# Kernel optimization log

Hardware: AMD Instinct MI355X
Metric: run time of the kernel (lower is better)

The kernel has to match this reference:

```python
import jax, jax.numpy as jnp
import numpy as np

B, H, W = 8, 64, 64
D = 256          # in_dim == key_dim == value_dim
HEADS = 8
DK = D // HEADS  # per-head channels (key == value)
EPS = 1e-5


def _ln(x, g, b):
    m = jnp.mean(x, axis=-1, keepdims=True)
    v = jnp.var(x, axis=-1, keepdims=True)
    return (x - m) * jax.lax.rsqrt(v + EPS) * g + b


def setup_inputs() -> dict:
    key = jax.random.key(0)
    ks = jax.random.split(key, 8)
    return {
        "x1": jax.random.normal(ks[0], (B, H, W, 2 * D), jnp.float32),
        "x2": jax.random.normal(ks[1], (B, H, W, D), jnp.float32),
        "linear_w": jax.random.normal(ks[2], (2 * D, D), jnp.float32) * 0.02,
        "linear_b": jax.random.normal(ks[3], (D,), jnp.float32) * 0.02,
        "ln1_g": jnp.ones((D,), jnp.float32) + jax.random.normal(ks[4], (D,), jnp.float32) * 0.02,
        "ln1_b": jax.random.normal(ks[5], (D,), jnp.float32) * 0.02,
        "reproj_w": jax.random.normal(ks[6], (2 * D, D), jnp.float32) * 0.02,  # 1x1 conv kernel [out,in]
        "reproj_b": jax.random.normal(ks[7], (2 * D,), jnp.float32) * 0.02,
        "ln_attn_g": jnp.ones((2 * D,), jnp.float32),
        "ln_attn_b": jnp.zeros((2 * D,), jnp.float32),
    }


def _cross_attention(n1, n2, reproj_w, reproj_b, ln_g, ln_b):
    # n1 (values source), n2 (keys/queries source): [B,H,W,D]
    N = H * W
    v = n1.reshape(B, N, D).transpose(0, 2, 1).reshape(B, HEADS, DK, N)
    kq = n2.reshape(B, N, D).transpose(0, 2, 1).reshape(B, HEADS, DK, N)
    k = jax.nn.softmax(kq, axis=-1)  # softmax over tokens (dim=2 in torch slice)
    q = jax.nn.softmax(kq, axis=2)   # softmax over per-head channels (dim=1 in torch slice)
    # attended[b,h,d,n] = sum_m sum_e q[b,h,d,m] k[b,h,e,m] v[b,h,e,n]
    ctx = jnp.einsum('bhdm,bhem->bhde', q, k)          # [B,h,dk,dk]
    att = jnp.einsum('bhde,bhen->bhdn', ctx, v)        # [B,h,dk,N]
    agg = att.reshape(B, D, H, W)                      # concat heads along channels
    rep = jnp.einsum('od,bdhw->bohw', reproj_w, agg) + reproj_b[None, :, None, None]
    rep = rep.transpose(0, 2, 3, 1)                    # [B,H,W,2D]
    return _ln(rep, ln_g, ln_b)


def reference(x1, x2, linear_w, linear_b, ln1_g, ln1_b, reproj_w, reproj_b, ln_attn_g, ln_attn_b):
    n1 = _ln(x1 @ linear_w + linear_b, ln1_g, ln1_b)   # [B,H,W,D]
    n2 = _ln(x2, ln1_g, ln1_b)                          # [B,H,W,D]
    attn = _cross_attention(n1, n2, reproj_w, reproj_b, ln_attn_g, ln_attn_b)
    return x1 + attn
```

## Files before the change

kernel.cpp:

```cpp
#include <hip/hip_runtime.h>
#include <stdint.h>

typedef __bf16 bf16x8 __attribute__((ext_vector_type(8)));
typedef float f32x4 __attribute__((ext_vector_type(4)));

#define EPS 1e-5f

__device__ __forceinline__ float b2f(unsigned short u) {
    union { unsigned int i; float f; } c; c.i = ((unsigned int)u) << 16; return c.f;
}
__device__ __forceinline__ unsigned short f2b(float f) {
    union { float f; unsigned int i; } c; c.f = f;
    unsigned int i = c.i;
    return (unsigned short)((i + 0x7FFFu + ((i >> 16) & 1u)) >> 16);
}

__global__ void k_zero(float* __restrict__ p, int n) {
    int i = blockIdx.x * 256 + threadIdx.x;
    if (i < n) p[i] = 0.0f;
}

__global__ void k_params(const float* __restrict__ lw, const float* __restrict__ rw,
                         const float* __restrict__ lb, const float* __restrict__ g1,
                         const float* __restrict__ b1, const float* __restrict__ rb,
                         const float* __restrict__ ga, const float* __restrict__ ba,
                         unsigned short* __restrict__ wt1,
                         unsigned short* __restrict__ rwb,
                         unsigned short* __restrict__ vec) {
    int gid = blockIdx.x * 256 + threadIdx.x;
    if (gid < 131072) {
        int k = gid >> 8, n = gid & 255;
        wt1[n * 512 + k] = f2b(lw[gid]);
    } else if (gid < 262144) {
        int j = gid - 131072;
        rwb[j] = f2b(rw[j]);
    } else if (gid < 264448) {
        int j = gid - 262144;
        if (j < 256)       vec[j] = f2b(lb[j]);
        else if (j < 512)  vec[j] = f2b(g1[j - 256]);
        else if (j < 768)  vec[j] = f2b(b1[j - 512]);
        else if (j < 1280) vec[j] = f2b(rb[j - 768]);
        else if (j < 1792) vec[j] = f2b(ga[j - 1280]);
        else               vec[j] = f2b(ba[j - 1792]);
    }
}

__global__ __launch_bounds__(256) void k_stats(const float* __restrict__ x2,
                                               float2* __restrict__ stats) {
    int t = threadIdx.x, lane = t & 63, w = t >> 6;
    size_t row = (size_t)blockIdx.x * 4 + w;
    float4 f = *(const float4*)(x2 + row * 256 + lane * 4);
    float s = f.x + f.y + f.z + f.w;
    float q = f.x * f.x + f.y * f.y + f.z * f.z + f.w * f.w;
#pragma unroll
    for (int msk = 1; msk < 64; msk <<= 1) {
        s += __shfl_xor(s, msk, 64);
        q += __shfl_xor(q, msk, 64);
    }
    float mn = s * (1.0f / 256.0f);
    float rstd = rsqrtf(q * (1.0f / 256.0f) - mn * mn + EPS);
    if (lane == 0) stats[row] = make_float2(mn, rstd);
}

__global__ __launch_bounds__(256) void k_ctx(const float* __restrict__ x2,
                                             const float2* __restrict__ stats,
                                             const unsigned short* __restrict__ vec,
                                             float* __restrict__ ctxraw) {
    __shared__ float E[64 * 36];
    __shared__ float Q[64 * 36];
    __shared__ float gs[32], bs[32];
    int bh = blockIdx.x >> 3;
    int b = bh >> 3, h = bh & 7;
    int ch = blockIdx.x & 7;
    int t = threadIdx.x;
    if (t < 32) { gs[t] = b2f(vec[256 + h * 32 + t]); bs[t] = b2f(vec[512 + h * 32 + t]); }
    __syncthreads();
    int d = t >> 3, e0 = (t & 7) * 4;
    float a0 = 0.f, a1 = 0.f, a2 = 0.f, a3 = 0.f;
    const float* base = x2 + ((size_t)b * 4096 + ch * 512) * 256 + h * 32;
    int srow = b * 4096 + ch * 512;
    const int m = t >> 2, c0 = (t & 3) * 8;
    for (int s0 = 0; s0 < 512; s0 += 64) {
        float2 st = stats[srow + s0 + m];
        const float4* p = (const float4*)(base + (size_t)(s0 + m) * 256 + c0);
        float4 f0 = p[0], f1 = p[1];
        float ev[8];
        ev[0] = __expf((f0.x - st.x) * st.y * gs[c0 + 0] + bs[c0 + 0]);
        ev[1] = __expf((f0.y - st.x) * st.y * gs[c0 + 1] + bs[c0 + 1]);
        ev[2] = __expf((f0.z - st.x) * st.y * gs[c0 + 2] + bs[c0 + 2]);
        ev[3] = __expf((f0.w - st.x) * st.y * gs[c0 + 3] + bs[c0 + 3]);
        ev[4] = __expf((f1.x - st.x) * st.y * gs[c0 + 4] + bs[c0 + 4]);
        ev[5] = __expf((f1.y - st.x) * st.y * gs[c0 + 5] + bs[c0 + 5]);
        ev[6] = __expf((f1.z - st.x) * st.y * gs[c0 + 6] + bs[c0 + 6]);
        ev[7] = __expf((f1.w - st.x) * st.y * gs[c0 + 7] + bs[c0 + 7]);
        float ps = ev[0] + ev[1] + ev[2] + ev[3] + ev[4] + ev[5] + ev[6] + ev[7];
        ps += __shfl_xor(ps, 1, 64);
        ps += __shfl_xor(ps, 2, 64);
        float qi = 1.0f / ps;
        *(float4*)(E + m * 36 + c0)     = make_float4(ev[0], ev[1], ev[2], ev[3]);
        *(float4*)(E + m * 36 + c0 + 4) = make_float4(ev[4], ev[5], ev[6], ev[7]);
        *(float4*)(Q + m * 36 + c0)     = make_float4(ev[0]*qi, ev[1]*qi, ev[2]*qi, ev[3]*qi);
        *(float4*)(Q + m * 36 + c0 + 4) = make_float4(ev[4]*qi, ev[5]*qi, ev[6]*qi, ev[7]*qi);
        __syncthreads();
#pragma unroll 4
        for (int mm = 0; mm < 64; mm++) {
            float qd = Q[mm * 36 + d];
            float4 e4 = *(const float4*)(E + mm * 36 + e0);
            a0 += qd * e4.x; a1 += qd * e4.y; a2 += qd * e4.z; a3 += qd * e4.w;
        }
        __syncthreads();
    }
    float* dst = ctxraw + ((size_t)bh << 10) + (d << 5) + e0;
    atomicAdd(dst + 0, a0);
    atomicAdd(dst + 1, a1);
    atomicAdd(dst + 2, a2);
    atomicAdd(dst + 3, a3);
}

__global__ __launch_bounds__(256) void k_w2(const float* __restrict__ ctxraw,
                                            const unsigned short* __restrict__ rwb,
                                            unsigned short* __restrict__ w2t) {
    __shared__ float ctx_s[1024];
    __shared__ float cinv[32];
    int blk = blockIdx.x;
    int b = blk >> 6, h = (blk >> 3) & 7, os = blk & 7;
    int bh = b * 8 + h;
    int t = threadIdx.x;
#pragma unroll
    for (int i = 0; i < 4; i++) ctx_s[t + 256 * i] = ctxraw[((size_t)bh << 10) + t + 256 * i];
    __syncthreads();
    if (t < 32) {
        float s = 0.f;
#pragma unroll
        for (int d = 0; d < 32; d++) s += ctx_s[d * 32 + t];
        cinv[t] = 1.0f / s;
    }
    __syncthreads();
    int o = os * 64 + (t >> 2);
    int e0 = (t & 3) * 8;
    float wv[32];
    const uint4* wp = (const uint4*)(rwb + (size_t)o * 256 + h * 32);
#pragma unroll
    for (int qd = 0; qd < 4; qd++) {
        uint4 u = wp[qd];
        unsigned int uu[4] = {u.x, u.y, u.z, u.w};
#pragma unroll
        for (int j = 0; j < 4; j++) {
            wv[qd * 8 + j * 2]     = b2f((unsigned short)(uu[j] & 0xFFFFu));
            wv[qd * 8 + j * 2 + 1] = b2f((unsigned short)(uu[j] >> 16));
        }
    }
    float s[8];
#pragma unroll
    for (int j = 0; j < 8; j++) s[j] = 0.f;
#pragma unroll 8
    for (int d = 0; d < 32; d++) {
        float w = wv[d];
#pragma unroll
        for (int j = 0; j < 8; j++) s[j] += ctx_s[d * 32 + e0 + j] * w;
    }
    ushort4 o4a, o4b;
    o4a.x = f2b(s[0] * cinv[e0 + 0]); o4a.y = f2b(s[1] * cinv[e0 + 1]);
    o4a.z = f2b(s[2] * cinv[e0 + 2]); o4a.w = f2b(s[3] * cinv[e0 + 3]);
    o4b.x = f2b(s[4] * cinv[e0 + 4]); o4b.y = f2b(s[5] * cinv[e0 + 5]);
    o4b.z = f2b(s[6] * cinv[e0 + 6]); o4b.w = f2b(s[7] * cinv[e0 + 7]);
    unsigned short* dst = w2t + ((size_t)b * 512 + o) * 256 + h * 32 + e0;
    *(ushort4*)dst = o4a;
    *(ushort4*)(dst + 4) = o4b;
}

__global__ __launch_bounds__(256) void k_gemm1(
    const float* __restrict__ x1, const unsigned short* __restrict__ wt1,
    const unsigned short* __restrict__ vec, unsigned short* __restrict__ n1) {
    __shared__ unsigned short pool[16896];
    unsigned short* As = pool;
    unsigned short* Bs = pool + 2560;
    unsigned short* n1s = pool;
    const int t = threadIdx.x;
    const int lane = t & 63, w = t >> 6;
    const int l15 = lane & 15, quad = lane >> 4;
    const int row0 = blockIdx.x * 64;
    const int mrow = (w << 4) + l15;
    const int k8 = quad * 8;
    const int stg_m = t >> 2, stg_k = (t & 3) * 8;

    f32x4 acc[16];
#pragma unroll
    for (int i = 0; i < 16; i++) acc[i] = (f32x4){0.f, 0.f, 0.f, 0.f};

    for (int k0 = 0; k0 < 512; k0 += 32) {
        {
            const float* xf = x1 + (size_t)(row0 + stg_m) * 512 + k0 + stg_k;
            float4 f0 = *(const float4*)xf;
            float4 f1 = *(const float4*)(xf + 4);
            ushort4 lo, hi;
            lo.x = f2b(f0.x); lo.y = f2b(f0.y); lo.z = f2b(f0.z); lo.w = f2b(f0.w);
            hi.x = f2b(f1.x); hi.y = f2b(f1.y); hi.z = f2b(f1.z); hi.w = f2b(f1.w);
            *(ushort4*)(As + stg_m * 40 + stg_k) = lo;
            *(ushort4*)(As + stg_m * 40 + stg_k + 4) = hi;
        }
#pragma unroll
        for (int p = 0; p < 4; p++) {
            int n = stg_m + p * 64;
            *(uint4*)(Bs + n * 40 + stg_k) =
                *(const uint4*)(wt1 + (size_t)n * 512 + k0 + stg_k);
        }
        __syncthreads();
        bf16x8 a = *(const bf16x8*)(As + mrow * 40 + k8);
#pragma unroll
        for (int cb = 0; cb < 16; cb++) {
            bf16x8 bf = *(const bf16x8*)(Bs + ((cb << 4) + l15) * 40 + k8);
            acc[cb] = __builtin_amdgcn_mfma_f32_16x16x32_bf16(a, bf, acc[cb], 0, 0, 0);
        }
        __syncthreads();
    }
#pragma unroll
    for (int cb = 0; cb < 16; cb++) {
        float bc = b2f(vec[(cb << 4) + l15]);
#pragma unroll
        for (int r = 0; r < 4; r++) acc[cb][r] += bc;
    }
    float mean_[4], rstd_[4];
#pragma unroll
    for (int r = 0; r < 4; r++) {
        float s = 0.f, q = 0.f;
#pragma unroll
        for (int cb = 0; cb < 16; cb++) { float v = acc[cb][r]; s += v; q += v * v; }
#pragma unroll
        for (int msk = 1; msk < 16; msk <<= 1) {
            s += __shfl_xor(s, msk, 64);
            q += __shfl_xor(q, msk, 64);
        }
        float mn = s * (1.0f / 256.0f);
        mean_[r] = mn;
        rstd_[r] = rsqrtf(q * (1.0f / 256.0f) - mn * mn + EPS);
    }
#pragma unroll
    for (int cb = 0; cb < 16; cb++) {
        int col = (cb << 4) + l15;
        float gg = b2f(vec[256 + col]), bbv = b2f(vec[512 + col]);
#pragma unroll
        for (int r = 0; r < 4; r++) {
            int rr = (w << 4) + (quad << 2) + r;
            n1s[rr * 264 + col] = f2b((acc[cb][r] - mean_[r]) * rstd_[r] * gg + bbv);
        }
    }
    __syncthreads();
    {
        int row = t >> 2;
        unsigned short* dst = n1 + (size_t)(row0 + row) * 256;
        const unsigned short* src = n1s + row * 264;
#pragma unroll
        for (int j = 0; j < 8; j++) {
            int chunk = (t & 3) * 8 + j;
            *(uint4*)(dst + chunk * 8) = *(const uint4*)(src + chunk * 8);
        }
    }
}

__global__ __launch_bounds__(512) void k_gemm2(
    const unsigned short* __restrict__ n1, const unsigned short* __restrict__ w2t,
    const unsigned short* __restrict__ vec, const float* __restrict__ x1,
    float* __restrict__ out) {
    __shared__ unsigned short As[64 * 40];
    __shared__ unsigned short Bs[512 * 40];
    __shared__ float2 red[2][64];
    const int t = threadIdx.x;
    const int lane = t & 63, w = t >> 6;
    const int l15 = lane & 15, quad = lane >> 4;
    const int hf = w >> 2, wr = w & 3;
    const int row0 = blockIdx.x * 64;
    const unsigned short* wb = w2t + (size_t)(row0 >> 12) * (512 * 256);
    const int mrow = (wr << 4) + l15;
    const int k8 = quad * 8;

    f32x4 acc[16];
#pragma unroll
    for (int i = 0; i < 16; i++) acc[i] = (f32x4){0.f, 0.f, 0.f, 0.f};

    for (int k0 = 0; k0 < 256; k0 += 32) {
        if (t < 256) {
            int m = t >> 2, kc = (t & 3) * 8;
            *(uint4*)(As + m * 40 + kc) =
                *(const uint4*)(n1 + (size_t)(row0 + m) * 256 + k0 + kc);
        }
#pragma unroll
        for (int p = 0; p < 4; p++) {
            int n = (t >> 2) + p * 128, kc = (t & 3) * 8;
            *(uint4*)(Bs + n * 40 + kc) =
                *(const uint4*)(wb + (size_t)n * 256 + k0 + kc);
        }
        __syncthreads();
        bf16x8 a = *(const bf16x8*)(As + mrow * 40 + k8);
#pragma unroll
        for (int cb = 0; cb < 16; cb++) {
            int ncol = (hf << 8) + (cb << 4) + l15;
            bf16x8 bf = *(const bf16x8*)(Bs + ncol * 40 + k8);
            acc[cb] = __builtin_amdgcn_mfma_f32_16x16x32_bf16(a, bf, acc[cb], 0, 0, 0);
        }
        __syncthreads();
    }
#pragma unroll
    for (int cb = 0; cb < 16; cb++) {
        float bc = b2f(vec[768 + (hf << 8) + (cb << 4) + l15]);
#pragma unroll
        for (int r = 0; r < 4; r++) acc[cb][r] += bc;
    }
#pragma unroll
    for (int r = 0; r < 4; r++) {
        float s = 0.f, q = 0.f;
#pragma unroll
        for (int cb = 0; cb < 16; cb++) { float v = acc[cb][r]; s += v; q += v * v; }
#pragma unroll
        for (int msk = 1; msk < 16; msk <<= 1) {
            s += __shfl_xor(s, msk, 64);
            q += __shfl_xor(q, msk, 64);
        }
        if (l15 == 0) red[hf][(wr << 4) + (quad << 2) + r] = make_float2(s, q);
    }
    __syncthreads();
    float mean_[4], rstd_[4];
#pragma unroll
    for (int r = 0; r < 4; r++) {
        int rl = (wr << 4) + (quad << 2) + r;
        float2 cA = red[0][rl], cB = red[1][rl];
        float s = cA.x + cB.x, q = cA.y + cB.y;
        float mn = s * (1.0f / 512.0f);
        mean_[r] = mn;
        rstd_[r] = rsqrtf(q * (1.0f / 512.0f) - mn * mn + EPS);
    }
#pragma unroll
    for (int cb = 0; cb < 16; cb++) {
        int col = (hf << 8) + (cb << 4) + l15;
        float gg = b2f(vec[1280 + col]), bbv = b2f(vec[1792 + col]);
#pragma unroll
        for (int r = 0; r < 4; r++) {
            size_t idx = (size_t)(row0 + (wr << 4) + (quad << 2) + r) * 512 + col;
            out[idx] = (acc[cb][r] - mean_[r]) * rstd_[r] * gg + bbv + x1[idx];
        }
    }
}

extern "C" void kernel_launch(void* const* d_in, const int* in_sizes, int n_in,
                              void* d_out, int out_size, void* d_ws, size_t ws_size,
                              hipStream_t stream) {
    const float* x1 = (const float*)d_in[0];
    const float* x2 = (const float*)d_in[1];
    const float* lw = (const float*)d_in[2];
    const float* lb = (const float*)d_in[3];
    const float* g1 = (const float*)d_in[4];
    const float* b1 = (const float*)d_in[5];
    const float* rw = (const float*)d_in[6];
    const float* rb = (const float*)d_in[7];
    const float* ga = (const float*)d_in[8];
    const float* ba = (const float*)d_in[9];
    float* out = (float*)d_out;

    char* ws = (char*)d_ws;
    float*          ctxr  = (float*)(ws);
    float2*         stats = (float2*)(ws + 262144);
    unsigned short* wt1   = (unsigned short*)(ws + 524288);
    unsigned short* rwb   = (unsigned short*)(ws + 786432);
    unsigned short* vec   = (unsigned short*)(ws + 1048576);
    unsigned short* w2t   = (unsigned short*)(ws + 1064960);
    unsigned short* n1    = (unsigned short*)(ws + 4194304);

    k_zero<<<dim3(256), dim3(256), 0, stream>>>(ctxr, 65536);
    k_params<<<dim3(1033), dim3(256), 0, stream>>>(lw, rw, lb, g1, b1, rb, ga, ba,
                                                   wt1, rwb, vec);
    k_stats<<<dim3(8192), dim3(256), 0, stream>>>(x2, stats);
    k_ctx<<<dim3(512), dim3(256), 0, stream>>>(x2, stats, vec, ctxr);
    k_w2<<<dim3(512), dim3(256), 0, stream>>>(ctxr, rwb, w2t);
    k_gemm1<<<dim3(512), dim3(256), 0, stream>>>(x1, wt1, vec, n1);
    k_gemm2<<<dim3(512), dim3(512), 0, stream>>>(n1, w2t, vec, x1, out);
}
```

Before: 244.0 us.

## Use MFMA for ctx, drop atomics, enlarge GEMM row tiles to 128

The ctx kernel now computes the per-head q·k^T product with 32x32x16 bf16 MFMA over token slabs instead of scalar FMAs. It writes per-chunk partial results that k_w2 sums, which removes the zero-fill kernel and the float atomics. Both GEMM kernels move to 128-row tiles with 512 threads, and gemm2 keeps the full 512-column row in one wave so the cross-wave LayerNorm reduction through shared memory is gone. The cost is bf16 rounding of the softmax terms in ctx and higher register pressure from 32 accumulators in gemm2.

```diff
diff --git a/kernel.cpp b/kernel.cpp
--- a/kernel.cpp
+++ b/kernel.cpp
@@ -3,6 +3,7 @@
 
 typedef __bf16 bf16x8 __attribute__((ext_vector_type(8)));
 typedef float f32x4 __attribute__((ext_vector_type(4)));
+typedef float f32x16 __attribute__((ext_vector_type(16)));
 
 #define EPS 1e-5f
 
@@ -13,11 +14,6 @@
     union { float f; unsigned int i; } c; c.f = f;
     unsigned int i = c.i;
     return (unsigned short)((i + 0x7FFFu + ((i >> 16) & 1u)) >> 16);
-}
-
-__global__ void k_zero(float* __restrict__ p, int n) {
-    int i = blockIdx.x * 256 + threadIdx.x;
-    if (i < n) p[i] = 0.0f;
 }
 
 __global__ void k_params(const float* __restrict__ lw, const float* __restrict__ rw,
@@ -65,59 +61,83 @@
 __global__ __launch_bounds__(256) void k_ctx(const float* __restrict__ x2,
                                              const float2* __restrict__ stats,
                                              const unsigned short* __restrict__ vec,
-                                             float* __restrict__ ctxraw) {
-    __shared__ float E[64 * 36];
-    __shared__ float Q[64 * 36];
-    __shared__ float gs[32], bs[32];
-    int bh = blockIdx.x >> 3;
-    int b = bh >> 3, h = bh & 7;
-    int ch = blockIdx.x & 7;
-    int t = threadIdx.x;
-    if (t < 32) { gs[t] = b2f(vec[256 + h * 32 + t]); bs[t] = b2f(vec[512 + h * 32 + t]); }
+                                             float* __restrict__ ctxr) {
+    __shared__ f32x4 pool4[1056];
+    unsigned short* E = (unsigned short*)pool4;
+    unsigned short* Q = E + 32 * 132;
+    float* Racc = (float*)pool4;
+
+    const int blk = blockIdx.x;
+    const int bh = blk >> 3, chunk = blk & 7;
+    const int b = bh >> 3, h = bh & 7;
+    const int t = threadIdx.x;
+    const int ch = t & 31, tk2 = t >> 5;
+    const int w = t >> 6, lane = t & 63;
+    const int khalf = lane >> 5, mn32 = lane & 31;
+
+    const float gch = b2f(vec[256 + h * 32 + ch]);
+    const float bch = b2f(vec[512 + h * 32 + ch]);
+    const int tokbase = b * 4096 + chunk * 512;
+    const float* xb = x2 + (size_t)tokbase * 256 + h * 32;
+
+    f32x16 acc = {};
+    for (int slab = 0; slab < 4; slab++) {
+#pragma unroll
+        for (int it = 0; it < 8; it++) {
+            int tl = it * 16 + tk2 * 2;
+            int tok = slab * 128 + tl;
+            float2 st0 = stats[tokbase + tok];
+            float2 st1 = stats[tokbase + tok + 1];
+            float xv0 = xb[(size_t)tok * 256 + ch];
+            float xv1 = xb[(size_t)(tok + 1) * 256 + ch];
+            float e0 = __expf((xv0 - st0.x) * st0.y * gch + bch);
+            float e1 = __expf((xv1 - st1.x) * st1.y * gch + bch);
+            float s0 = e0, s1 = e1;
+#pragma unroll
+            for (int msk = 1; msk < 32; msk <<= 1) {
+                s0 += __shfl_xor(s0, msk, 64);
+                s1 += __shfl_xor(s1, msk, 64);
+            }
+            float qi0 = 1.0f / s0, qi1 = 1.0f / s1;
+            unsigned int pe = (unsigned int)f2b(e0) | ((unsigned int)f2b(e1) << 16);
+            unsigned int pq = (unsigned int)f2b(e0 * qi0) | ((unsigned int)f2b(e1 * qi1) << 16);
+            *(unsigned int*)(E + ch * 132 + tl) = pe;
+            *(unsigned int*)(Q + ch * 132 + tl) = pq;
+        }
+        __syncthreads();
+#pragma unroll
+        for (int k16 = 0; k16 < 2; k16++) {
+            int off = mn32 * 132 + w * 32 + k16 * 16 + khalf * 8;
+            union { bf16x8 v; uint2 u[2]; } fa, fb;
+            fa.u[0] = *(const uint2*)(Q + off);
+            fa.u[1] = *(const uint2*)(Q + off + 4);
+            fb.u[0] = *(const uint2*)(E + off);
+            fb.u[1] = *(const uint2*)(E + off + 4);
+            acc = __builtin_amdgcn_mfma_f32_32x32x16_bf16(fa.v, fb.v, acc, 0, 0, 0);
+        }
+        __syncthreads();
+    }
+    {
+        float* R = Racc + w * 1024;
+#pragma unroll
+        for (int j = 0; j < 16; j++) {
+            int row = (j & 3) + 8 * (j >> 2) + 4 * khalf;
+            R[row * 32 + mn32] = acc[j];
+        }
+    }
     __syncthreads();
-    int d = t >> 3, e0 = (t & 7) * 4;
-    float a0 = 0.f, a1 = 0.f, a2 = 0.f, a3 = 0.f;
-    const float* base = x2 + ((size_t)b * 4096 + ch * 512) * 256 + h * 32;
-    int srow = b * 4096 + ch * 512;
-    const int m = t >> 2, c0 = (t & 3) * 8;
-    for (int s0 = 0; s0 < 512; s0 += 64) {
-        float2 st = stats[srow + s0 + m];
-        const float4* p = (const float4*)(base + (size_t)(s0 + m) * 256 + c0);
-        float4 f0 = p[0], f1 = p[1];
-        float ev[8];
-        ev[0] = __expf((f0.x - st.x) * st.y * gs[c0 + 0] + bs[c0 + 0]);
-        ev[1] = __expf((f0.y - st.x) * st.y * gs[c0 + 1] + bs[c0 + 1]);
-        ev[2] = __expf((f0.z - st.x) * st.y * gs[c0 + 2] + bs[c0 + 2]);
-        ev[3] = __expf((f0.w - st.x) * st.y * gs[c0 + 3] + bs[c0 + 3]);
-        ev[4] = __expf((f1.x - st.x) * st.y * gs[c0 + 4] + bs[c0 + 4]);
-        ev[5] = __expf((f1.y - st.x) * st.y * gs[c0 + 5] + bs[c0 + 5]);
-        ev[6] = __expf((f1.z - st.x) * st.y * gs[c0 + 6] + bs[c0 + 6]);
-        ev[7] = __expf((f1.w - st.x) * st.y * gs[c0 + 7] + bs[c0 + 7]);
-        float ps = ev[0] + ev[1] + ev[2] + ev[3] + ev[4] + ev[5] + ev[6] + ev[7];
-        ps += __shfl_xor(ps, 1, 64);
-        ps += __shfl_xor(ps, 2, 64);
-        float qi = 1.0f / ps;
-        *(float4*)(E + m * 36 + c0)     = make_float4(ev[0], ev[1], ev[2], ev[3]);
-        *(float4*)(E + m * 36 + c0 + 4) = make_float4(ev[4], ev[5], ev[6], ev[7]);
-        *(float4*)(Q + m * 36 + c0)     = make_float4(ev[0]*qi, ev[1]*qi, ev[2]*qi, ev[3]*qi);
-        *(float4*)(Q + m * 36 + c0 + 4) = make_float4(ev[4]*qi, ev[5]*qi, ev[6]*qi, ev[7]*qi);
-        __syncthreads();
-#pragma unroll 4
-        for (int mm = 0; mm < 64; mm++) {
-            float qd = Q[mm * 36 + d];
-            float4 e4 = *(const float4*)(E + mm * 36 + e0);
-            a0 += qd * e4.x; a1 += qd * e4.y; a2 += qd * e4.z; a3 += qd * e4.w;
-        }
-        __syncthreads();
-    }
-    float* dst = ctxraw + ((size_t)bh << 10) + (d << 5) + e0;
-    atomicAdd(dst + 0, a0);
-    atomicAdd(dst + 1, a1);
-    atomicAdd(dst + 2, a2);
-    atomicAdd(dst + 3, a3);
-}
-
-__global__ __launch_bounds__(256) void k_w2(const float* __restrict__ ctxraw,
+    {
+        float4 s = make_float4(0.f, 0.f, 0.f, 0.f);
+#pragma unroll
+        for (int ww = 0; ww < 4; ww++) {
+            float4 v = *(const float4*)(Racc + ww * 1024 + t * 4);
+            s.x += v.x; s.y += v.y; s.z += v.z; s.w += v.w;
+        }
+        *(float4*)(ctxr + ((size_t)(bh * 8 + chunk) << 10) + t * 4) = s;
+    }
+}
+
+__global__ __launch_bounds__(256) void k_w2(const float* __restrict__ ctxr,
                                             const unsigned short* __restrict__ rwb,
                                             unsigned short* __restrict__ w2t) {
     __shared__ float ctx_s[1024];
@@ -127,7 +147,13 @@
     int bh = b * 8 + h;
     int t = threadIdx.x;
 #pragma unroll
-    for (int i = 0; i < 4; i++) ctx_s[t + 256 * i] = ctxraw[((size_t)bh << 10) + t + 256 * i];
+    for (int i = 0; i < 4; i++) {
+        float s = 0.f;
+#pragma unroll
+        for (int c = 0; c < 8; c++)
+            s += ctxr[((size_t)(bh * 8 + c) << 10) + t + 256 * i];
+        ctx_s[t + 256 * i] = s;
+    }
     __syncthreads();
     if (t < 32) {
         float s = 0.f;
@@ -169,20 +195,20 @@
     *(ushort4*)(dst + 4) = o4b;
 }
 
-__global__ __launch_bounds__(256) void k_gemm1(
+__global__ __launch_bounds__(512, 2) void k_gemm1(
     const float* __restrict__ x1, const unsigned short* __restrict__ wt1,
     const unsigned short* __restrict__ vec, unsigned short* __restrict__ n1) {
-    __shared__ unsigned short pool[16896];
-    unsigned short* As = pool;
-    unsigned short* Bs = pool + 2560;
-    unsigned short* n1s = pool;
+    __shared__ f32x4 pool4[2112];
+    unsigned short* As = (unsigned short*)pool4;
+    unsigned short* Bs = As + 128 * 40;
+    unsigned short* n1s = (unsigned short*)pool4;
     const int t = threadIdx.x;
     const int lane = t & 63, w = t >> 6;
     const int l15 = lane & 15, quad = lane >> 4;
-    const int row0 = blockIdx.x * 64;
-    const int mrow = (w << 4) + l15;
+    const int row0 = blockIdx.x * 128;
+    const int mrow = w * 16 + l15;
     const int k8 = quad * 8;
-    const int stg_m = t >> 2, stg_k = (t & 3) * 8;
+    const int sm = t >> 2, sk = (t & 3) * 8;
 
     f32x4 acc[16];
 #pragma unroll
@@ -190,27 +216,27 @@
 
     for (int k0 = 0; k0 < 512; k0 += 32) {
         {
-            const float* xf = x1 + (size_t)(row0 + stg_m) * 512 + k0 + stg_k;
+            const float* xf = x1 + (size_t)(row0 + sm) * 512 + k0 + sk;
             float4 f0 = *(const float4*)xf;
             float4 f1 = *(const float4*)(xf + 4);
             ushort4 lo, hi;
             lo.x = f2b(f0.x); lo.y = f2b(f0.y); lo.z = f2b(f0.z); lo.w = f2b(f0.w);
             hi.x = f2b(f1.x); hi.y = f2b(f1.y); hi.z = f2b(f1.z); hi.w = f2b(f1.w);
-            *(ushort4*)(As + stg_m * 40 + stg_k) = lo;
-            *(ushort4*)(As + stg_m * 40 + stg_k + 4) = hi;
-        }
-#pragma unroll
-        for (int p = 0; p < 4; p++) {
-            int n = stg_m + p * 64;
-            *(uint4*)(Bs + n * 40 + stg_k) =
-                *(const uint4*)(wt1 + (size_t)n * 512 + k0 + stg_k);
+            *(ushort4*)(As + sm * 40 + sk) = lo;
+            *(ushort4*)(As + sm * 40 + sk + 4) = hi;
+        }
+#pragma unroll
+        for (int p = 0; p < 2; p++) {
+            int n = sm + p * 128;
+            *(uint4*)(Bs + n * 40 + sk) =
+                *(const uint4*)(wt1 + (size_t)n * 512 + k0 + sk);
         }
         __syncthreads();
         bf16x8 a = *(const bf16x8*)(As + mrow * 40 + k8);
 #pragma unroll
         for (int cb = 0; cb < 16; cb++) {
-            bf16x8 bf = *(const bf16x8*)(Bs + ((cb << 4) + l15) * 40 + k8);
-            acc[cb] = __builtin_amdgcn_mfma_f32_16x16x32_bf16(a, bf, acc[cb], 0, 0, 0);
+            bf16x8 bm = *(const bf16x8*)(Bs + ((cb << 4) + l15) * 40 + k8);
+            acc[cb] = __builtin_amdgcn_mfma_f32_16x16x32_bf16(a, bm, acc[cb], 0, 0, 0);
         }
         __syncthreads();
     }
@@ -231,111 +257,102 @@
             s += __shfl_xor(s, msk, 64);
             q += __shfl_xor(q, msk, 64);
         }
-        float mn = s * (1.0f / 256.0f);
-        mean_[r] = mn;
-        rstd_[r] = rsqrtf(q * (1.0f / 256.0f) - mn * mn + EPS);
-    }
-#pragma unroll
-    for (int cb = 0; cb < 16; cb++) {
-        int col = (cb << 4) + l15;
-        float gg = b2f(vec[256 + col]), bbv = b2f(vec[512 + col]);
-#pragma unroll
-        for (int r = 0; r < 4; r++) {
-            int rr = (w << 4) + (quad << 2) + r;
-            n1s[rr * 264 + col] = f2b((acc[cb][r] - mean_[r]) * rstd_[r] * gg + bbv);
-        }
-    }
-    __syncthreads();
-    {
-        int row = t >> 2;
-        unsigned short* dst = n1 + (size_t)(row0 + row) * 256;
-        const unsigned short* src = n1s + row * 264;
-#pragma unroll
-        for (int j = 0; j < 8; j++) {
-            int chunk = (t & 3) * 8 + j;
-            *(uint4*)(dst + chunk * 8) = *(const uint4*)(src + chunk * 8);
-        }
-    }
-}
-
-__global__ __launch_bounds__(512) void k_gemm2(
+        float mv = s * (1.0f / 256.0f);
+        mean_[r] = mv;
+        rstd_[r] = rsqrtf(q * (1.0f / 256.0f) - mv * mv + EPS);
+    }
+#pragma unroll
+    for (int half = 0; half < 2; half++) {
+        if ((w >> 2) == half) {
+            int rbase = (w & 3) * 16 + (quad << 2);
+#pragma unroll
+            for (int cb = 0; cb < 16; cb++) {
+                int col = (cb << 4) + l15;
+                float gg = b2f(vec[256 + col]), bbv = b2f(vec[512 + col]);
+#pragma unroll
+                for (int r = 0; r < 4; r++)
+                    n1s[(rbase + r) * 264 + col] =
+                        f2b((acc[cb][r] - mean_[r]) * rstd_[r] * gg + bbv);
+            }
+        }
+        __syncthreads();
+        {
+            int rr = t >> 3, cc = (t & 7) * 32;
+            const unsigned short* src = n1s + rr * 264 + cc;
+            unsigned short* dst = n1 + (size_t)(row0 + half * 64 + rr) * 256 + cc;
+#pragma unroll
+            for (int j = 0; j < 4; j++)
+                *(uint4*)(dst + j * 8) = *(const uint4*)(src + j * 8);
+        }
+        __syncthreads();
+    }
+}
+
+__global__ __launch_bounds__(512, 2) void k_gemm2(
     const unsigned short* __restrict__ n1, const unsigned short* __restrict__ w2t,
     const unsigned short* __restrict__ vec, const float* __restrict__ x1,
     float* __restrict__ out) {
-    __shared__ unsigned short As[64 * 40];
+    __shared__ unsigned short As[128 * 40];
     __shared__ unsigned short Bs[512 * 40];
-    __shared__ float2 red[2][64];
     const int t = threadIdx.x;
     const int lane = t & 63, w = t >> 6;
     const int l15 = lane & 15, quad = lane >> 4;
-    const int hf = w >> 2, wr = w & 3;
-    const int row0 = blockIdx.x * 64;
+    const int row0 = blockIdx.x * 128;
     const unsigned short* wb = w2t + (size_t)(row0 >> 12) * (512 * 256);
-    const int mrow = (wr << 4) + l15;
+    const int mrow = w * 16 + l15;
     const int k8 = quad * 8;
-
-    f32x4 acc[16];
-#pragma unroll
-    for (int i = 0; i < 16; i++) acc[i] = (f32x4){0.f, 0.f, 0.f, 0.f};
+    const int sm = t >> 2, sk = (t & 3) * 8;
+
+    f32x4 acc[32];
+#pragma unroll
+    for (int i = 0; i < 32; i++) acc[i] = (f32x4){0.f, 0.f, 0.f, 0.f};
 
     for (int k0 = 0; k0 < 256; k0 += 32) {
-        if (t < 256) {
-            int m = t >> 2, kc = (t & 3) * 8;
-            *(uint4*)(As + m * 40 + kc) =
-                *(const uint4*)(n1 + (size_t)(row0 + m) * 256 + k0 + kc);
-        }
+        *(uint4*)(As + sm * 40 + sk) =
+            *(const uint4*)(n1 + (size_t)(row0 + sm) * 256 + k0 + sk);
 #pragma unroll
         for (int p = 0; p < 4; p++) {
-            int n = (t >> 2) + p * 128, kc = (t & 3) * 8;
-            *(uint4*)(Bs + n * 40 + kc) =
-                *(const uint4*)(wb + (size_t)n * 256 + k0 + kc);
+            int n = sm + p * 128;
+            *(uint4*)(Bs + n * 40 + sk) =
+                *(const uint4*)(wb + (size_t)n * 256 + k0 + sk);
         }
         __syncthreads();
         bf16x8 a = *(const bf16x8*)(As + mrow * 40 + k8);
 #pragma unroll
-        for (int cb = 0; cb < 16; cb++) {
-            int ncol = (hf << 8) + (cb << 4) + l15;
-            bf16x8 bf = *(const bf16x8*)(Bs + ncol * 40 + k8);
-            acc[cb] = __builtin_amdgcn_mfma_f32_16x16x32_bf16(a, bf, acc[cb], 0, 0, 0);
-        }
-        __syncthreads();
-    }
-#pragma unroll
-    for (int cb = 0; cb < 16; cb++) {
-        float bc = b2f(vec[768 + (hf << 8) + (cb << 4) + l15]);
+        for (int cb = 0; cb < 32; cb++) {
+            bf16x8 bm = *(const bf16x8*)(Bs + ((cb << 4) + l15) * 40 + k8);
+            acc[cb] = __builtin_amdgcn_mfma_f32_16x16x32_bf16(a, bm, acc[cb], 0, 0, 0);
+        }
+        __syncthreads();
+    }
+#pragma unroll
+    for (int cb = 0; cb < 32; cb++) {
+        float bc = b2f(vec[768 + (cb << 4) + l15]);
 #pragma unroll
         for (int r = 0; r < 4; r++) acc[cb][r] += bc;
     }
+    float mean_[4], rstd_[4];
 #pragma unroll
     for (int r = 0; r < 4; r++) {
         float s = 0.f, q = 0.f;
 #pragma unroll
-        for (int cb = 0; cb < 16; cb++) { float v = acc[cb][r]; s += v; q += v * v; }
+        for (int cb = 0; cb < 32; cb++) { float v = acc[cb][r]; s += v; q += v * v; }
 #pragma unroll
         for (int msk = 1; msk < 16; msk <<= 1) {
             s += __shfl_xor(s, msk, 64);
             q += __shfl_xor(q, msk, 64);
         }
-        if (l15 == 0) red[hf][(wr << 4) + (quad << 2) + r] = make_float2(s, q);
-    }
-    __syncthreads();
-    float mean_[4], rstd_[4];
-#pragma unroll
-    for (int r = 0; r < 4; r++) {
-        int rl = (wr << 4) + (quad << 2) + r;
-        float2 cA = red[0][rl], cB = red[1][rl];
-        float s = cA.x + cB.x, q = cA.y + cB.y;
-        float mn = s * (1.0f / 512.0f);
-        mean_[r] = mn;
-        rstd_[r] = rsqrtf(q * (1.0f / 512.0f) - mn * mn + EPS);
-    }
-#pragma unroll
-    for (int cb = 0; cb < 16; cb++) {
-        int col = (hf << 8) + (cb << 4) + l15;
+        float mv = s * (1.0f / 512.0f);
+        mean_[r] = mv;
+        rstd_[r] = rsqrtf(q * (1.0f / 512.0f) - mv * mv + EPS);
+    }
+#pragma unroll
+    for (int cb = 0; cb < 32; cb++) {
+        int col = (cb << 4) + l15;
         float gg = b2f(vec[1280 + col]), bbv = b2f(vec[1792 + col]);
 #pragma unroll
         for (int r = 0; r < 4; r++) {
-            size_t idx = (size_t)(row0 + (wr << 4) + (quad << 2) + r) * 512 + col;
+            size_t idx = (size_t)(row0 + w * 16 + (quad << 2) + r) * 512 + col;
             out[idx] = (acc[cb][r] - mean_[r]) * rstd_[r] * gg + bbv + x1[idx];
         }
     }
@@ -358,19 +375,18 @@
 
     char* ws = (char*)d_ws;
     float*          ctxr  = (float*)(ws);
-    float2*         stats = (float2*)(ws + 262144);
-    unsigned short* wt1   = (unsigned short*)(ws + 524288);
-    unsigned short* rwb   = (unsigned short*)(ws + 786432);
-    unsigned short* vec   = (unsigned short*)(ws + 1048576);
-    unsigned short* w2t   = (unsigned short*)(ws + 1064960);
-    unsigned short* n1    = (unsigned short*)(ws + 4194304);
-
-    k_zero<<<dim3(256), dim3(256), 0, stream>>>(ctxr, 65536);
+    float2*         stats = (float2*)(ws + 2097152);
+    unsigned short* wt1   = (unsigned short*)(ws + 2359296);
+    unsigned short* rwb   = (unsigned short*)(ws + 2621440);
+    unsigned short* vec   = (unsigned short*)(ws + 2883584);
+    unsigned short* w2t   = (unsigned short*)(ws + 2891776);
+    unsigned short* n1    = (unsigned short*)(ws + 4988928);
+
     k_params<<<dim3(1033), dim3(256), 0, stream>>>(lw, rw, lb, g1, b1, rb, ga, ba,
                                                    wt1, rwb, vec);
     k_stats<<<dim3(8192), dim3(256), 0, stream>>>(x2, stats);
     k_ctx<<<dim3(512), dim3(256), 0, stream>>>(x2, stats, vec, ctxr);
     k_w2<<<dim3(512), dim3(256), 0, stream>>>(ctxr, rwb, w2t);
-    k_gemm1<<<dim3(512), dim3(256), 0, stream>>>(x1, wt1, vec, n1);
-    k_gemm2<<<dim3(512), dim3(512), 0, stream>>>(n1, w2t, vec, x1, out);
-}
+    k_gemm1<<<dim3(256), dim3(512), 0, stream>>>(x1, wt1, vec, n1);
+    k_gemm2<<<dim3(256), dim3(512), 0, stream>>>(n1, w2t, vec, x1, out);
+}
```

Result: slower. 265.9 us (+9.0%).
